# Performance work log

Measured on AMD Instinct MI355X. Metric: run time of the kernel, lower is better.

Reference implementation:

```python
import jax, jax.numpy as jnp
import numpy as np

B, QLEN, MLEN, E, H, DH = 2, 1024, 1024, 1024, 16, 64
KLEN = QLEN + MLEN
LN_EPS = 1e-3  # keras LayerNormalization default epsilon


def layer_norm(x, gamma, beta):
    mu = jnp.mean(x, axis=-1, keepdims=True)
    var = jnp.mean(jnp.square(x - mu), axis=-1, keepdims=True)
    return (x - mu) * jax.lax.rsqrt(var + LN_EPS) * gamma + beta


def rel_shift(x):
    # x: [B, H, q, k] -> standard Transformer-XL relative shift
    b, h, q, k = x.shape
    x = jnp.pad(x, ((0, 0), (0, 0), (0, 0), (1, 0)))
    x = x.reshape(b, h, k + 1, q)[:, :, 1:, :]
    return x.reshape(b, h, q, k)


def setup_inputs() -> dict:
    key = jax.random.key(0)
    ks = jax.random.split(key, 12)
    s = 0.02
    inp = {
        "w": jax.random.normal(ks[0], (B, QLEN, E), jnp.float32),
        "r": jax.random.normal(ks[1], (1, KLEN, E), jnp.float32),
        "member": jax.random.normal(ks[2], (B, MLEN, E), jnp.float32),
        # causal mask over concatenated keys: 1 = masked
        "attn_mask": (jnp.arange(KLEN)[None, :] > (jnp.arange(QLEN)[:, None] + MLEN)).astype(jnp.float32),
        "Wq": jax.random.normal(ks[3], (E, H * DH), jnp.float32) * s,
        "Wk": jax.random.normal(ks[4], (E, H * DH), jnp.float32) * s,
        "Wv": jax.random.normal(ks[5], (E, H * DH), jnp.float32) * s,
        "Wr": jax.random.normal(ks[6], (E, H * DH), jnp.float32) * s,
        "Wo": jax.random.normal(ks[7], (H * DH, E), jnp.float32) * s,
        "r_w_bias": jnp.zeros((H, DH), jnp.float32),
        "r_r_bias": jnp.zeros((H, DH), jnp.float32),
        "ln1_g": jnp.ones((E,), jnp.float32),
        "ln1_b": jnp.zeros((E,), jnp.float32),
        "W1": jax.random.normal(ks[8], (E, 4 * E), jnp.float32) * s,
        "W2": jax.random.normal(ks[9], (4 * E, E), jnp.float32) * s,
        "ln2_g": jnp.ones((E,), jnp.float32),
        "ln2_b": jnp.zeros((E,), jnp.float32),
    }
    return inp


def reference(w, r, member, attn_mask, Wq, Wk, Wv, Wr, Wo, r_w_bias, r_r_bias,
              ln1_g, ln1_b, W1, W2, ln2_g, ln2_b):
    b, qlen, e = w.shape
    h, dh = r_w_bias.shape
    cat = jnp.concatenate([member, w], axis=1)          # [B, klen, E]
    q = (cat @ Wq)[:, -qlen:]                           # [B, q, H*DH]
    k = cat @ Wk                                        # [B, klen, H*DH]
    v = cat @ Wv
    rp = (r @ Wr)[0]                                    # [klen, H*DH] (shared over batch)
    qh = q.reshape(b, qlen, h, dh)
    kh = k.reshape(b, -1, h, dh)
    vh = v.reshape(b, -1, h, dh)
    rh = rp.reshape(-1, h, dh)
    AC = jnp.einsum('bqhd,bkhd->bhqk', qh + r_w_bias, kh)
    BD = jnp.einsum('bqhd,khd->bhqk', qh + r_r_bias, rh)
    BD = rel_shift(BD)
    attn = (AC + BD) / jnp.sqrt(jnp.float32(e))         # note: scaled by sqrt(embed_size)
    m = attn_mask[None, None]                           # [1,1,q,klen]
    attn = attn * (1.0 - m) - 1e30 * m
    p = jax.nn.softmax(attn, axis=-1)
    o = jnp.einsum('bhqk,bkhd->bqhd', p, vh).reshape(b, qlen, h * dh)
    o = o @ Wo
    x = layer_norm(w + o, ln1_g, ln1_b)
    y = jax.nn.relu(x @ W1) @ W2
    return layer_norm(y + x, ln2_g, ln2_b)
```

## Files before the change

### kernel.cpp

```cpp
#include <hip/hip_runtime.h>
#include <hip/hip_bf16.h>
#include <stdint.h>

typedef __bf16 bf16x8 __attribute__((ext_vector_type(8)));
typedef float  f32x4  __attribute__((ext_vector_type(4)));

constexpr int BB   = 2;
constexpr int QL   = 1024;
constexpr int ML   = 1024;
constexpr int KL   = 2048;
constexpr int ED   = 1024;
constexpr int HH   = 16;
constexpr int FF   = 4096;
constexpr size_t MN = 2048u * 1024u;

__device__ __forceinline__ bf16x8 ld8(const __hip_bfloat16* p) {
    return *reinterpret_cast<const bf16x8*>(p);
}
__device__ __forceinline__ void st8(__hip_bfloat16* p, bf16x8 v) {
    *reinterpret_cast<bf16x8*>(p) = v;
}
__device__ __forceinline__ f32x4 mfma16(bf16x8 a, bf16x8 b, f32x4 c) {
    return __builtin_amdgcn_mfma_f32_16x16x32_bf16(a, b, c, 0, 0, 0);
}
__device__ __forceinline__ void async16(void* lds, const void* g) {
    __builtin_amdgcn_global_load_lds((__attribute__((address_space(1))) void*)g,
                                     (__attribute__((address_space(3))) void*)lds,
                                     16, 0, 0);
}

__global__ __launch_bounds__(256) void build_cat_r(const float* __restrict__ w,
                                                   const float* __restrict__ mem,
                                                   const float* __restrict__ r,
                                                   __hip_bfloat16* __restrict__ cat,
                                                   __hip_bfloat16* __restrict__ rbf) {
    const int bx = blockIdx.x;
    const float* src;
    __hip_bfloat16* dst;
    size_t g;
    if (bx < 2048) {
        size_t t = (size_t)bx * 256 + threadIdx.x;
        g = t * 8;
        int b   = (int)(g >> 21);
        int rem = (int)(g & ((1u << 21) - 1));
        int j = rem >> 10, e = rem & 1023;
        src = (j < ML) ? &mem[((size_t)b * ML + j) * ED + e]
                       : &w[((size_t)b * QL + (j - ML)) * ED + e];
        dst = &cat[g];
    } else {
        g = ((size_t)(bx - 2048) * 256 + threadIdx.x) * 8;
        src = &r[g];
        dst = &rbf[g];
    }
    float4 f0 = *(const float4*)src;
    float4 f1 = *(const float4*)(src + 4);
    union { bf16x8 v; __hip_bfloat16 h[8]; } u;
    u.h[0] = __float2bfloat16(f0.x); u.h[1] = __float2bfloat16(f0.y);
    u.h[2] = __float2bfloat16(f0.z); u.h[3] = __float2bfloat16(f0.w);
    u.h[4] = __float2bfloat16(f1.x); u.h[5] = __float2bfloat16(f1.y);
    u.h[6] = __float2bfloat16(f1.z); u.h[7] = __float2bfloat16(f1.w);
    st8(dst, u.v);
}

__global__ __launch_bounds__(256) void transpose_cast(const float* __restrict__ in,
                                                      __hip_bfloat16* __restrict__ out,
                                                      int K, int N) {
    __shared__ float tile[32][33];
    const int tx = threadIdx.x & 31, ty = threadIdx.x >> 5;
    const int n0 = blockIdx.x * 32, k0 = blockIdx.y * 32;
#pragma unroll
    for (int i = 0; i < 4; ++i)
        tile[ty + i * 8][tx] = in[(size_t)(k0 + ty + i * 8) * N + n0 + tx];
    __syncthreads();
#pragma unroll
    for (int i = 0; i < 4; ++i)
        out[(size_t)(n0 + ty + i * 8) * K + k0 + tx] = __float2bfloat16(tile[tx][ty + i * 8]);
}

__global__ __launch_bounds__(256) void tc5(const float* __restrict__ s0, const float* __restrict__ s1,
                                           const float* __restrict__ s2, const float* __restrict__ s3,
                                           const float* __restrict__ s4,
                                           __hip_bfloat16* __restrict__ wqkvT,
                                           __hip_bfloat16* __restrict__ wot) {
    __shared__ float tile[32][33];
    const int z = blockIdx.z;
    const float* in = (z == 0) ? s0 : (z == 1) ? s1 : (z == 2) ? s2 : (z == 3) ? s3 : s4;
    __hip_bfloat16* out = (z == 4) ? wot : wqkvT + (size_t)z * 1024 * 1024;
    const int tx = threadIdx.x & 31, ty = threadIdx.x >> 5;
    const int n0 = blockIdx.x * 32, k0 = blockIdx.y * 32;
#pragma unroll
    for (int i = 0; i < 4; ++i)
        tile[ty + i * 8][tx] = in[(size_t)(k0 + ty + i * 8) * 1024 + n0 + tx];
    __syncthreads();
#pragma unroll
    for (int i = 0; i < 4; ++i)
        out[(size_t)(n0 + ty + i * 8) * 1024 + k0 + tx] = __float2bfloat16(tile[tx][ty + i * 8]);
}

__global__ __launch_bounds__(256) void transpose_v(const __hip_bfloat16* __restrict__ v,
                                                   __hip_bfloat16* __restrict__ vt) {
    __shared__ __hip_bfloat16 tile[32][33];
    const int tx = threadIdx.x & 31, ty = threadIdx.x >> 5;
    const int s = blockIdx.z, b = s >> 4, h = s & 15;
    const int j0 = blockIdx.x * 32, d0 = blockIdx.y * 32;
#pragma unroll
    for (int i = 0; i < 4; ++i)
        tile[ty + i * 8][tx] =
            v[((size_t)b * KL + j0 + ty + i * 8) * 1024 + h * 64 + d0 + tx];
    __syncthreads();
#pragma unroll
    for (int i = 0; i < 4; ++i)
        vt[((size_t)s * 64 + d0 + ty + i * 8) * KL + j0 + tx] = tile[tx][ty + i * 8];
}

template <int EPI, bool SK>
__global__ __launch_bounds__(256) void gemm_bt(const __hip_bfloat16* __restrict__ A,
                                               const __hip_bfloat16* __restrict__ Bt,
                                               void* __restrict__ Cv,
                                               int N, int kLen, int lda, int ldb) {
    __shared__ __align__(16) __hip_bfloat16 sA[128 * 32];
    __shared__ __align__(16) __hip_bfloat16 sB[128 * 32];
    const int tid = threadIdx.x;
    const int lane = tid & 63;
    const int l16 = lane & 15, quad = lane >> 4;
    const int wv = tid >> 6;
    const int wm = wv >> 1, wn = wv & 1;
    const int bm = blockIdx.y * 128, bn = blockIdx.x * 128;
    const int kOff = SK ? blockIdx.z * kLen : 0;
    const int c0 = tid, c1 = 256 + tid;
    const int r0 = c0 >> 2, o0 = (c0 & 3) * 8;
    const int r1 = c1 >> 2, o1 = (c1 & 3) * 8;
    f32x4 acc[4][4] = {};
    for (int k0 = 0; k0 < kLen; k0 += 32) {
        async16(&sA[c0 * 8], A + (size_t)(bm + r0) * lda + kOff + k0 + o0);
        async16(&sA[c1 * 8], A + (size_t)(bm + r1) * lda + kOff + k0 + o1);
        async16(&sB[c0 * 8], Bt + (size_t)(bn + r0) * ldb + kOff + k0 + o0);
        async16(&sB[c1 * 8], Bt + (size_t)(bn + r1) * ldb + kOff + k0 + o1);
        __syncthreads();
        bf16x8 af[4], bfr[4];
#pragma unroll
        for (int i = 0; i < 4; ++i)
            af[i] = ld8(&sA[(wm * 64 + i * 16 + l16) * 32 + quad * 8]);
#pragma unroll
        for (int j = 0; j < 4; ++j)
            bfr[j] = ld8(&sB[(wn * 64 + j * 16 + l16) * 32 + quad * 8]);
#pragma unroll
        for (int i = 0; i < 4; ++i)
#pragma unroll
            for (int j = 0; j < 4; ++j)
                acc[i][j] = mfma16(af[i], bfr[j], acc[i][j]);
        __syncthreads();
    }
#pragma unroll
    for (int i = 0; i < 4; ++i)
#pragma unroll
        for (int j = 0; j < 4; ++j)
#pragma unroll
            for (int rg = 0; rg < 4; ++rg) {
                size_t row = bm + wm * 64 + i * 16 + quad * 4 + rg;
                size_t col = bn + wn * 64 + j * 16 + l16;
                float v = acc[i][j][rg];
                if (EPI == 0) {
                    float* C = (float*)Cv + (SK ? (size_t)blockIdx.z * MN : 0);
                    C[row * N + col] = v;
                } else {
                    __hip_bfloat16* C = (__hip_bfloat16*)Cv;
                    C[row * N + col] = __float2bfloat16(fmaxf(v, 0.f));
                }
            }
}

__global__ __launch_bounds__(256) void gemm_qkvr(const __hip_bfloat16* __restrict__ cat,
                                                 const __hip_bfloat16* __restrict__ rbf,
                                                 const __hip_bfloat16* __restrict__ Bt,
                                                 __hip_bfloat16* __restrict__ qwb,
                                                 __hip_bfloat16* __restrict__ qrb,
                                                 __hip_bfloat16* __restrict__ kbuf,
                                                 __hip_bfloat16* __restrict__ vbuf,
                                                 __hip_bfloat16* __restrict__ rpb,
                                                 const float* __restrict__ rwb,
                                                 const float* __restrict__ rrb) {
    const int bm = blockIdx.y * 128, bn = blockIdx.x * 128;
    const int region = blockIdx.x >> 3;
    if (region == 0 && (bm & 2047) < 1024) return;
    if (region == 3 && bm >= 2048) return;
    const __hip_bfloat16* A = (region == 3) ? rbf : cat;
    __shared__ __align__(16) __hip_bfloat16 sA[128 * 32];
    __shared__ __align__(16) __hip_bfloat16 sB[128 * 32];
    const int tid = threadIdx.x;
    const int lane = tid & 63;
    const int l16 = lane & 15, quad = lane >> 4;
    const int wv = tid >> 6;
    const int wm = wv >> 1, wn = wv & 1;
    const int c0 = tid, c1 = 256 + tid;
    const int r0 = c0 >> 2, o0 = (c0 & 3) * 8;
    const int r1 = c1 >> 2, o1 = (c1 & 3) * 8;
    f32x4 acc[4][4] = {};
    for (int k0 = 0; k0 < 1024; k0 += 32) {
        async16(&sA[c0 * 8], A + (size_t)(bm + r0) * 1024 + k0 + o0);
        async16(&sA[c1 * 8], A + (size_t)(bm + r1) * 1024 + k0 + o1);
        async16(&sB[c0 * 8], Bt + (size_t)(bn + r0) * 1024 + k0 + o0);
        async16(&sB[c1 * 8], Bt + (size_t)(bn + r1) * 1024 + k0 + o1);
        __syncthreads();
        bf16x8 af[4], bfr[4];
#pragma unroll
        for (int i = 0; i < 4; ++i)
            af[i] = ld8(&sA[(wm * 64 + i * 16 + l16) * 32 + quad * 8]);
#pragma unroll
        for (int j = 0; j < 4; ++j)
            bfr[j] = ld8(&sB[(wn * 64 + j * 16 + l16) * 32 + quad * 8]);
#pragma unroll
        for (int i = 0; i < 4; ++i)
#pragma unroll
            for (int j = 0; j < 4; ++j)
                acc[i][j] = mfma16(af[i], bfr[j], acc[i][j]);
        __syncthreads();
    }
#pragma unroll
    for (int j = 0; j < 4; ++j) {
        const int col = bn + wn * 64 + j * 16 + l16;
        float bw = 0.f, br = 0.f;
        if (region == 0) { bw = rwb[col]; br = rrb[col]; }
#pragma unroll
        for (int i = 0; i < 4; ++i)
#pragma unroll
            for (int rg = 0; rg < 4; ++rg) {
                const int row = bm + wm * 64 + i * 16 + quad * 4 + rg;
                const int bb = row >> 11, jr = row & 2047;
                float v = acc[i][j][rg];
                if (region == 0) {
                    size_t o = ((size_t)(bb * 1024 + (jr - 1024))) * 1024 + col;
                    qwb[o] = __float2bfloat16(v + bw);
                    qrb[o] = __float2bfloat16(v + br);
                } else if (region == 1) {
                    kbuf[((size_t)(bb * 2048 + jr)) * 1024 + (col - 1024)] = __float2bfloat16(v);
                } else if (region == 2) {
                    vbuf[((size_t)(bb * 2048 + jr)) * 1024 + (col - 2048)] = __float2bfloat16(v);
                } else {
                    rpb[(size_t)row * 1024 + (col - 3072)] = __float2bfloat16(v);
                }
            }
    }
}

__global__ __launch_bounds__(64, 3) void flash_attn5(
        const __hip_bfloat16* __restrict__ qw, const __hip_bfloat16* __restrict__ qr,
        const __hip_bfloat16* __restrict__ kbuf, const __hip_bfloat16* __restrict__ vtb,
        const __hip_bfloat16* __restrict__ rpb,
        float* __restrict__ Opart, float* __restrict__ lpart) {
    __shared__ __align__(16) __hip_bfloat16 spb[32][76];
    const int lane = threadIdx.x;
    const int l16 = lane & 15, quad = lane >> 4;
    const int id    = blockIdx.x;
    const int xcd   = id & 7;
    const int rest  = id >> 3;
    const int grp   = rest >> 7;
    const int local = rest & 127;
    const int p     = grp * 8 + xcd;
    const int b = p >> 4, h = p & 15;
    const int qi = local >> 2, chunk = local & 3;
    const int i0 = qi * 32;

    bf16x8 qaw[2][2], qar[2][2];
#pragma unroll
    for (int g = 0; g < 2; ++g)
#pragma unroll
        for (int kf = 0; kf < 2; ++kf) {
            size_t qi_ = ((size_t)(b * QL + i0 + g * 16 + l16)) * 1024 + h * 64 + kf * 32 + quad * 8;
            qaw[g][kf] = ld8(&qw[qi_]);
            qar[g][kf] = ld8(&qr[qi_]);
        }
    f32x4 oacc[2][4] = {};
    f32x4 lacc[2] = {};
    union { bf16x8 v; __hip_bfloat16 h8[8]; } ou;
#pragma unroll
    for (int j = 0; j < 8; ++j) ou.h8[j] = __float2bfloat16(l16 == 0 ? 1.f : 0.f);
    const bf16x8 onesf = ou.v;

    int srcIdx[4], selr[4];
#pragma unroll
    for (int r = 0; r < 4; ++r) {
        int s = l16 + 15 - (quad * 4 + r);
        selr[r] = s >> 4;
        srcIdx[r] = (quad * 16) | (s & 15);
    }
    const int T = (i0 + 1119) >> 6;
    const int t0 = (chunk * T) >> 2, t1 = ((chunk + 1) * T) >> 2;
    const __hip_bfloat16* kB = kbuf + (size_t)b * KL * 1024 + h * 64;
    const __hip_bfloat16* vB = vtb + ((size_t)(b * HH + h) * 64) * 2048;
    const __hip_bfloat16* rB = rpb + h * 64;

    for (int jt = t0; jt < t1; ++jt) {
        const int j0 = jt * 64;
        f32x4 sfr[2][4];
#pragma unroll
        for (int nt = 0; nt < 4; ++nt) {
            const __hip_bfloat16* kr = kB + (size_t)(j0 + nt * 16 + l16) * 1024 + quad * 8;
            bf16x8 b0 = ld8(kr);
            bf16x8 b1 = ld8(kr + 32);
#pragma unroll
            for (int g = 0; g < 2; ++g) {
                f32x4 z = {};
                z = mfma16(qaw[g][0], b0, z);
                z = mfma16(qaw[g][1], b1, z);
                sfr[g][nt] = z;
            }
        }
        f32x4 bd[2][5];
        const int ubase = j0 - i0 + 992;
#pragma unroll
        for (int s = 0; s < 6; ++s) {
            int row = ubase + s * 16 + l16;
            if (row > 2047) row = 2047;
            const __hip_bfloat16* rr = rB + (size_t)row * 1024 + quad * 8;
            bf16x8 f0 = ld8(rr);
            bf16x8 f1 = ld8(rr + 32);
            if (s >= 1) {
                f32x4 z = {};
                z = mfma16(qar[0][0], f0, z);
                z = mfma16(qar[0][1], f1, z);
                bd[0][s - 1] = z;
            }
            if (s <= 4) {
                f32x4 z = {};
                z = mfma16(qar[1][0], f0, z);
                z = mfma16(qar[1][1], f1, z);
                bd[1][s] = z;
            }
        }
#pragma unroll
        for (int g = 0; g < 2; ++g) {
            float pre[5][4];
#pragma unroll
            for (int t = 0; t < 5; ++t)
#pragma unroll
                for (int r = 0; r < 4; ++r)
                    pre[t][r] = __shfl(bd[g][t][r], srcIdx[r], 64);
#pragma unroll
            for (int nt = 0; nt < 4; ++nt)
#pragma unroll
                for (int r = 0; r < 4; ++r) {
                    float bdv = selr[r] ? pre[nt + 1][r] : pre[nt][r];
                    float sv = (sfr[g][nt][r] + bdv) * 0.03125f;
                    int ii = i0 + g * 16 + quad * 4 + r;
                    int jj = j0 + nt * 16 + l16;
                    float p_ = (jj <= ii + ML) ? __expf(sv) : 0.f;
                    spb[g * 16 + quad * 4 + r][nt * 16 + l16] = __float2bfloat16(p_);
                }
        }
        bf16x8 pa[2][2];
#pragma unroll
        for (int g = 0; g < 2; ++g) {
            pa[g][0] = ld8(&spb[g * 16 + l16][quad * 8]);
            pa[g][1] = ld8(&spb[g * 16 + l16][32 + quad * 8]);
            lacc[g] = mfma16(pa[g][0], onesf, lacc[g]);
            lacc[g] = mfma16(pa[g][1], onesf, lacc[g]);
        }
#pragma unroll
        for (int dt = 0; dt < 4; ++dt) {
            const __hip_bfloat16* vr = vB + (size_t)(dt * 16 + l16) * 2048 + j0 + quad * 8;
            bf16x8 v0 = ld8(vr);
            bf16x8 v1 = ld8(vr + 32);
#pragma unroll
            for (int g = 0; g < 2; ++g) {
                oacc[g][dt] = mfma16(pa[g][0], v0, oacc[g][dt]);
                oacc[g][dt] = mfma16(pa[g][1], v1, oacc[g][dt]);
            }
        }
    }
    const size_t obase = ((size_t)((chunk * 2 + b) * HH + h)) * (1024 * 64);
#pragma unroll
    for (int g = 0; g < 2; ++g)
#pragma unroll
        for (int dt = 0; dt < 4; ++dt)
#pragma unroll
            for (int r = 0; r < 4; ++r) {
                int q = i0 + g * 16 + quad * 4 + r;
                Opart[obase + (size_t)q * 64 + dt * 16 + l16] = oacc[g][dt][r];
            }
    if (l16 == 0) {
        const size_t lbase = ((size_t)((chunk * 2 + b) * HH + h)) * 1024;
#pragma unroll
        for (int g = 0; g < 2; ++g)
#pragma unroll
            for (int r = 0; r < 4; ++r) {
                int q = i0 + g * 16 + quad * 4 + r;
                lpart[lbase + q] = lacc[g][r];
            }
    }
}

__global__ __launch_bounds__(256) void combine_attn(const float* __restrict__ Opart,
                                                    const float* __restrict__ lpart,
                                                    __hip_bfloat16* __restrict__ og) {
    size_t t = (size_t)blockIdx.x * 256 + threadIdx.x;
    size_t e4 = t * 4;
    int d  = (int)(e4 & 63);
    int q  = (int)((e4 >> 6) & 1023);
    int hh = (int)((e4 >> 16) & 15);
    int bb = (int)(e4 >> 20);
    float ox = 0.f, oy = 0.f, oz = 0.f, ow = 0.f, l = 0.f;
#pragma unroll
    for (int c = 0; c < 4; ++c) {
        size_t gsel = (size_t)((c * 2 + bb) * HH + hh);
        float4 o = *(const float4*)&Opart[gsel * (1024 * 64) + (size_t)q * 64 + d];
        ox += o.x; oy += o.y; oz += o.z; ow += o.w;
        l += lpart[gsel * 1024 + q];
    }
    float inv = 1.f / l;
    union { __hip_bfloat16 h[4]; uint2 u; } o;
    o.h[0] = __float2bfloat16(ox * inv);
    o.h[1] = __float2bfloat16(oy * inv);
    o.h[2] = __float2bfloat16(oz * inv);
    o.h[3] = __float2bfloat16(ow * inv);
    *(uint2*)&og[((size_t)bb * 1024 + q) * 1024 + hh * 64 + d] = o.u;
}

template <int NP, bool WB>
__global__ __launch_bounds__(256) void add_ln_k(const float* __restrict__ res,
                                                const float* __restrict__ parts,
                                                const float* __restrict__ gam,
                                                const float* __restrict__ bet,
                                                float* __restrict__ of,
                                                __hip_bfloat16* __restrict__ ob) {
    const int tid = threadIdx.x;
    const size_t base = (size_t)blockIdx.x * ED;
    const int col = tid * 4;
    float4 va = *(const float4*)&res[base + col];
    float x0 = va.x, x1 = va.y, x2 = va.z, x3 = va.w;
#pragma unroll
    for (int z = 0; z < NP; ++z) {
        float4 p = *(const float4*)&parts[(size_t)z * MN + base + col];
        x0 += p.x; x1 += p.y; x2 += p.z; x3 += p.w;
    }
    float s1 = x0 + x1 + x2 + x3;
    float s2 = x0 * x0 + x1 * x1 + x2 * x2 + x3 * x3;
    for (int o = 32; o > 0; o >>= 1) {
        s1 += __shfl_down(s1, o, 64);
        s2 += __shfl_down(s2, o, 64);
    }
    __shared__ float p1[4], p2[4];
    if ((tid & 63) == 0) { p1[tid >> 6] = s1; p2[tid >> 6] = s2; }
    __syncthreads();
    float S1 = p1[0] + p1[1] + p1[2] + p1[3];
    float S2 = p2[0] + p2[1] + p2[2] + p2[3];
    float mu = S1 * (1.0f / ED);
    float var = S2 * (1.0f / ED) - mu * mu;
    float rs = rsqrtf(var + 1e-3f);
    float4 g4 = *(const float4*)&gam[col];
    float4 b4 = *(const float4*)&bet[col];
    float y0 = (x0 - mu) * rs * g4.x + b4.x;
    float y1 = (x1 - mu) * rs * g4.y + b4.y;
    float y2 = (x2 - mu) * rs * g4.z + b4.z;
    float y3 = (x3 - mu) * rs * g4.w + b4.w;
    *(float4*)&of[base + col] = make_float4(y0, y1, y2, y3);
    if (WB) {
        ob[base + col + 0] = __float2bfloat16(y0);
        ob[base + col + 1] = __float2bfloat16(y1);
        ob[base + col + 2] = __float2bfloat16(y2);
        ob[base + col + 3] = __float2bfloat16(y3);
    }
}

extern "C" void kernel_launch(void* const* d_in, const int* in_sizes, int n_in,
                              void* d_out, int out_size, void* d_ws, size_t ws_size,
                              hipStream_t stream) {
    const float* w   = (const float*)d_in[0];
    const float* r   = (const float*)d_in[1];
    const float* mem = (const float*)d_in[2];
    const float* Wq  = (const float*)d_in[4];
    const float* Wk  = (const float*)d_in[5];
    const float* Wv  = (const float*)d_in[6];
    const float* Wr  = (const float*)d_in[7];
    const float* Wo  = (const float*)d_in[8];
    const float* rwb = (const float*)d_in[9];
    const float* rrb = (const float*)d_in[10];
    const float* g1  = (const float*)d_in[11];
    const float* b1  = (const float*)d_in[12];
    const float* W1  = (const float*)d_in[13];
    const float* W2  = (const float*)d_in[14];
    const float* g2  = (const float*)d_in[15];
    const float* b2  = (const float*)d_in[16];

    char* ws = (char*)d_ws;
    size_t off = 0;
    auto alloc = [&](size_t bytes) -> void* {
        void* p = ws + off;
        off += (bytes + 255) & ~(size_t)255;
        return p;
    };
    __hip_bfloat16* wqkvT = (__hip_bfloat16*)alloc((size_t)4096 * 1024 * 2);
    __hip_bfloat16* wot   = (__hip_bfloat16*)alloc((size_t)ED * ED * 2);
    __hip_bfloat16* w1t   = (__hip_bfloat16*)alloc((size_t)FF * ED * 2);
    __hip_bfloat16* w2t   = (__hip_bfloat16*)alloc((size_t)ED * FF * 2);
    __hip_bfloat16* qwb   = (__hip_bfloat16*)alloc((size_t)BB * QL * ED * 2);
    __hip_bfloat16* qrb   = (__hip_bfloat16*)alloc((size_t)BB * QL * ED * 2);
    __hip_bfloat16* vtb   = (__hip_bfloat16*)alloc((size_t)BB * KL * ED * 2);
    __hip_bfloat16* rpb   = (__hip_bfloat16*)alloc((size_t)KL * ED * 2);
    __hip_bfloat16* og    = (__hip_bfloat16*)alloc((size_t)BB * QL * ED * 2);
    char* regA = (char*)alloc((size_t)BB * KL * ED * 2);
    __hip_bfloat16* cat = (__hip_bfloat16*)regA;
    float*          xf  = (float*)regA;
    char* regB = (char*)alloc((size_t)KL * ED * 2);
    __hip_bfloat16* rbf = (__hip_bfloat16*)regB;
    __hip_bfloat16* xb  = (__hip_bfloat16*)regB;
    char* regC = (char*)alloc((size_t)BB * QL * FF * 2);
    __hip_bfloat16* kbuf = (__hip_bfloat16*)regC;
    __hip_bfloat16* vbuf = (__hip_bfloat16*)(regC + (size_t)BB * KL * ED * 2);
    __hip_bfloat16* y1   = (__hip_bfloat16*)regC;
    const size_t opartBytes = (size_t)8 * HH * QL * 64 * 4;
    const size_t lpartBytes = (size_t)8 * HH * QL * 4;
    size_t regEsz = opartBytes + lpartBytes;
    if (regEsz < (size_t)4 * MN * 4) regEsz = (size_t)4 * MN * 4;
    char* regE = (char*)alloc(regEsz);
    float* Opart  = (float*)regE;
    float* lpart  = (float*)(regE + opartBytes);
    float* o_part = (float*)regE;
    float* f_part = (float*)regE;
    if (off > ws_size) return;

    build_cat_r<<<3072, 256, 0, stream>>>(w, mem, r, cat, rbf);
    tc5<<<dim3(32, 32, 5), 256, 0, stream>>>(Wq, Wk, Wv, Wr, Wo, wqkvT, wot);
    transpose_cast<<<dim3(128, 32), 256, 0, stream>>>(W1, w1t, 1024, 4096);
    transpose_cast<<<dim3(32, 128), 256, 0, stream>>>(W2, w2t, 4096, 1024);

    gemm_qkvr<<<dim3(32, 32), 256, 0, stream>>>(cat, rbf, wqkvT, qwb, qrb, kbuf, vbuf, rpb,
                                                rwb, rrb);
    transpose_v<<<dim3(64, 2, 32), 256, 0, stream>>>(vbuf, vtb);

    flash_attn5<<<dim3(4096), 64, 0, stream>>>(qwb, qrb, kbuf, vtb, rpb, Opart, lpart);
    combine_attn<<<2048, 256, 0, stream>>>(Opart, lpart, og);

    gemm_bt<0, true><<<dim3(8, 16, 4), 256, 0, stream>>>(og, wot, o_part, 1024, 256, 1024, 1024);
    add_ln_k<4, true><<<2048, 256, 0, stream>>>(w, o_part, g1, b1, xf, xb);

    gemm_bt<2, false><<<dim3(32, 16, 1), 256, 0, stream>>>(xb, w1t, y1, 4096, 1024, 1024, 1024);
    gemm_bt<0, true><<<dim3(8, 16, 4), 256, 0, stream>>>(y1, w2t, f_part, 1024, 1024, 4096, 4096);
    add_ln_k<4, false><<<2048, 256, 0, stream>>>(xf, f_part, g2, b2, (float*)d_out, nullptr);
}
```

Measured before the change: 454.0 us.

## Share K and relative-position tiles in LDS across two waves in flash attention

The attention kernel now runs two waves per block, each handling 32 query rows of a 64-row block. The K tile and a 128-row relative-position window are staged cooperatively in shared memory, so both waves reuse them instead of each loading from global memory. The key-range split drops from four chunks to two, which halves the partial outputs the combine step has to merge. The cost is two block-wide barriers per tile, fewer and larger blocks, and more shared memory per block, which may lower occupancy.

Result: no change. 461.0 us (+1.5%).

```diff
diff --git a/kernel.cpp b/kernel.cpp
--- a/kernel.cpp
+++ b/kernel.cpp
@@ -243,32 +243,34 @@
     }
 }
 
-__global__ __launch_bounds__(64, 3) void flash_attn5(
+__global__ __launch_bounds__(128, 2) void flash_attn6(
         const __hip_bfloat16* __restrict__ qw, const __hip_bfloat16* __restrict__ qr,
         const __hip_bfloat16* __restrict__ kbuf, const __hip_bfloat16* __restrict__ vtb,
         const __hip_bfloat16* __restrict__ rpb,
         float* __restrict__ Opart, float* __restrict__ lpart) {
-    __shared__ __align__(16) __hip_bfloat16 spb[32][76];
-    const int lane = threadIdx.x;
+    __shared__ __align__(16) __hip_bfloat16 sk[64][72];
+    __shared__ __align__(16) __hip_bfloat16 srp[128][72];
+    __shared__ __align__(16) __hip_bfloat16 spb[2][32][72];
+    const int tid = threadIdx.x, wv = tid >> 6, lane = tid & 63;
     const int l16 = lane & 15, quad = lane >> 4;
     const int id    = blockIdx.x;
     const int xcd   = id & 7;
     const int rest  = id >> 3;
-    const int grp   = rest >> 7;
-    const int local = rest & 127;
+    const int grp   = rest >> 5;
+    const int local = rest & 31;
     const int p     = grp * 8 + xcd;
     const int b = p >> 4, h = p & 15;
-    const int qi = local >> 2, chunk = local & 3;
-    const int i0 = qi * 32;
+    const int qb = local >> 1, chunk = local & 1;
+    const int i0b = qb * 64, i0w = i0b + wv * 32;
 
     bf16x8 qaw[2][2], qar[2][2];
 #pragma unroll
     for (int g = 0; g < 2; ++g)
 #pragma unroll
         for (int kf = 0; kf < 2; ++kf) {
-            size_t qi_ = ((size_t)(b * QL + i0 + g * 16 + l16)) * 1024 + h * 64 + kf * 32 + quad * 8;
-            qaw[g][kf] = ld8(&qw[qi_]);
-            qar[g][kf] = ld8(&qr[qi_]);
+            size_t qi = ((size_t)(b * QL + i0w + g * 16 + l16)) * 1024 + h * 64 + kf * 32 + quad * 8;
+            qaw[g][kf] = ld8(&qw[qi]);
+            qar[g][kf] = ld8(&qr[qi]);
         }
     f32x4 oacc[2][4] = {};
     f32x4 lacc[2] = {};
@@ -282,22 +284,45 @@
     for (int r = 0; r < 4; ++r) {
         int s = l16 + 15 - (quad * 4 + r);
         selr[r] = s >> 4;
-        srcIdx[r] = (quad * 16) | (s & 15);
-    }
-    const int T = (i0 + 1119) >> 6;
-    const int t0 = (chunk * T) >> 2, t1 = ((chunk + 1) * T) >> 2;
-    const __hip_bfloat16* kB = kbuf + (size_t)b * KL * 1024 + h * 64;
-    const __hip_bfloat16* vB = vtb + ((size_t)(b * HH + h) * 64) * 2048;
-    const __hip_bfloat16* rB = rpb + h * 64;
+        srcIdx[r] = (lane & 48) | (s & 15);
+    }
+    const int T = qb + 17, Ta = T >> 1;
+    const int t0 = chunk ? Ta : 0, t1 = chunk ? T : Ta;
+    const int rbase = 32 - wv * 32;
 
     for (int jt = t0; jt < t1; ++jt) {
         const int j0 = jt * 64;
+        const int ub = j0 - i0b + 960;
+#pragma unroll
+        for (int pp = 0; pp < 4; ++pp) {
+            int cc = pp * 128 + tid, row = cc >> 3, off = (cc & 7) * 8;
+            st8(&sk[row][off], ld8(&kbuf[((size_t)(b * KL + j0 + row)) * 1024 + h * 64 + off]));
+        }
+#pragma unroll
+        for (int pp = 0; pp < 8; ++pp) {
+            int cc = pp * 128 + tid, row = cc >> 3, off = (cc & 7) * 8;
+            int u = ub + row;
+            if (u < KL) {
+                st8(&srp[row][off], ld8(&rpb[(size_t)u * 1024 + h * 64 + off]));
+            } else {
+                union { bf16x8 v; uint32_t w[4]; } z;
+                z.w[0] = z.w[1] = z.w[2] = z.w[3] = 0u;
+                st8(&srp[row][off], z.v);
+            }
+        }
+        bf16x8 vvf[4][2];
+#pragma unroll
+        for (int dt = 0; dt < 4; ++dt) {
+            size_t vr = ((size_t)((b * HH + h) * 64 + dt * 16 + l16)) * 2048 + j0 + quad * 8;
+            vvf[dt][0] = ld8(&vtb[vr]);
+            vvf[dt][1] = ld8(&vtb[vr + 32]);
+        }
+        __syncthreads();
         f32x4 sfr[2][4];
 #pragma unroll
         for (int nt = 0; nt < 4; ++nt) {
-            const __hip_bfloat16* kr = kB + (size_t)(j0 + nt * 16 + l16) * 1024 + quad * 8;
-            bf16x8 b0 = ld8(kr);
-            bf16x8 b1 = ld8(kr + 32);
+            bf16x8 b0 = ld8(&sk[nt * 16 + l16][quad * 8]);
+            bf16x8 b1 = ld8(&sk[nt * 16 + l16][32 + quad * 8]);
 #pragma unroll
             for (int g = 0; g < 2; ++g) {
                 f32x4 z = {};
@@ -306,67 +331,55 @@
                 sfr[g][nt] = z;
             }
         }
-        f32x4 bd[2][5];
-        const int ubase = j0 - i0 + 992;
-#pragma unroll
-        for (int s = 0; s < 6; ++s) {
-            int row = ubase + s * 16 + l16;
-            if (row > 2047) row = 2047;
-            const __hip_bfloat16* rr = rB + (size_t)row * 1024 + quad * 8;
-            bf16x8 f0 = ld8(rr);
-            bf16x8 f1 = ld8(rr + 32);
-            if (s >= 1) {
+        bf16x8 bF0[6], bF1[6];
+#pragma unroll
+        for (int t = 0; t < 6; ++t) {
+            int rr = rbase + t * 16 + l16;
+            bF0[t] = ld8(&srp[rr][quad * 8]);
+            bF1[t] = ld8(&srp[rr][32 + quad * 8]);
+        }
+#pragma unroll
+        for (int g = 0; g < 2; ++g) {
+            f32x4 bd[5];
+#pragma unroll
+            for (int t = 0; t < 5; ++t) {
+                int ts = t + 1 - g;
                 f32x4 z = {};
-                z = mfma16(qar[0][0], f0, z);
-                z = mfma16(qar[0][1], f1, z);
-                bd[0][s - 1] = z;
-            }
-            if (s <= 4) {
-                f32x4 z = {};
-                z = mfma16(qar[1][0], f0, z);
-                z = mfma16(qar[1][1], f1, z);
-                bd[1][s] = z;
-            }
-        }
-#pragma unroll
-        for (int g = 0; g < 2; ++g) {
+                z = mfma16(qar[g][0], bF0[ts], z);
+                z = mfma16(qar[g][1], bF1[ts], z);
+                bd[t] = z;
+            }
             float pre[5][4];
 #pragma unroll
             for (int t = 0; t < 5; ++t)
 #pragma unroll
                 for (int r = 0; r < 4; ++r)
-                    pre[t][r] = __shfl(bd[g][t][r], srcIdx[r], 64);
+                    pre[t][r] = __shfl(bd[t][r], srcIdx[r], 64);
 #pragma unroll
             for (int nt = 0; nt < 4; ++nt)
 #pragma unroll
                 for (int r = 0; r < 4; ++r) {
                     float bdv = selr[r] ? pre[nt + 1][r] : pre[nt][r];
                     float sv = (sfr[g][nt][r] + bdv) * 0.03125f;
-                    int ii = i0 + g * 16 + quad * 4 + r;
+                    int ii = i0w + g * 16 + quad * 4 + r;
                     int jj = j0 + nt * 16 + l16;
                     float p_ = (jj <= ii + ML) ? __expf(sv) : 0.f;
-                    spb[g * 16 + quad * 4 + r][nt * 16 + l16] = __float2bfloat16(p_);
+                    spb[wv][g * 16 + quad * 4 + r][nt * 16 + l16] = __float2bfloat16(p_);
                 }
         }
-        bf16x8 pa[2][2];
 #pragma unroll
         for (int g = 0; g < 2; ++g) {
-            pa[g][0] = ld8(&spb[g * 16 + l16][quad * 8]);
-            pa[g][1] = ld8(&spb[g * 16 + l16][32 + quad * 8]);
-            lacc[g] = mfma16(pa[g][0], onesf, lacc[g]);
-            lacc[g] = mfma16(pa[g][1], onesf, lacc[g]);
-        }
-#pragma unroll
-        for (int dt = 0; dt < 4; ++dt) {
-            const __hip_bfloat16* vr = vB + (size_t)(dt * 16 + l16) * 2048 + j0 + quad * 8;
-            bf16x8 v0 = ld8(vr);
-            bf16x8 v1 = ld8(vr + 32);
-#pragma unroll
-            for (int g = 0; g < 2; ++g) {
-                oacc[g][dt] = mfma16(pa[g][0], v0, oacc[g][dt]);
-                oacc[g][dt] = mfma16(pa[g][1], v1, oacc[g][dt]);
-            }
-        }
+            bf16x8 pa0 = ld8(&spb[wv][g * 16 + l16][quad * 8]);
+            bf16x8 pa1 = ld8(&spb[wv][g * 16 + l16][32 + quad * 8]);
+            lacc[g] = mfma16(pa0, onesf, lacc[g]);
+            lacc[g] = mfma16(pa1, onesf, lacc[g]);
+#pragma unroll
+            for (int dt = 0; dt < 4; ++dt) {
+                oacc[g][dt] = mfma16(pa0, vvf[dt][0], oacc[g][dt]);
+                oacc[g][dt] = mfma16(pa1, vvf[dt][1], oacc[g][dt]);
+            }
+        }
+        __syncthreads();
     }
     const size_t obase = ((size_t)((chunk * 2 + b) * HH + h)) * (1024 * 64);
 #pragma unroll
@@ -375,7 +388,7 @@
         for (int dt = 0; dt < 4; ++dt)
 #pragma unroll
             for (int r = 0; r < 4; ++r) {
-                int q = i0 + g * 16 + quad * 4 + r;
+                int q = i0w + g * 16 + quad * 4 + r;
                 Opart[obase + (size_t)q * 64 + dt * 16 + l16] = oacc[g][dt][r];
             }
     if (l16 == 0) {
@@ -384,7 +397,7 @@
         for (int g = 0; g < 2; ++g)
 #pragma unroll
             for (int r = 0; r < 4; ++r) {
-                int q = i0 + g * 16 + quad * 4 + r;
+                int q = i0w + g * 16 + quad * 4 + r;
                 lpart[lbase + q] = lacc[g][r];
             }
     }
@@ -401,7 +414,7 @@
     int bb = (int)(e4 >> 20);
     float ox = 0.f, oy = 0.f, oz = 0.f, ow = 0.f, l = 0.f;
 #pragma unroll
-    for (int c = 0; c < 4; ++c) {
+    for (int c = 0; c < 2; ++c) {
         size_t gsel = (size_t)((c * 2 + bb) * HH + hh);
         float4 o = *(const float4*)&Opart[gsel * (1024 * 64) + (size_t)q * 64 + d];
         ox += o.x; oy += o.y; oz += o.z; ow += o.w;
@@ -508,8 +521,8 @@
     __hip_bfloat16* kbuf = (__hip_bfloat16*)regC;
     __hip_bfloat16* vbuf = (__hip_bfloat16*)(regC + (size_t)BB * KL * ED * 2);
     __hip_bfloat16* y1   = (__hip_bfloat16*)regC;
-    const size_t opartBytes = (size_t)8 * HH * QL * 64 * 4;
-    const size_t lpartBytes = (size_t)8 * HH * QL * 4;
+    const size_t opartBytes = (size_t)4 * HH * QL * 64 * 4;
+    const size_t lpartBytes = (size_t)4 * HH * QL * 4;
     size_t regEsz = opartBytes + lpartBytes;
     if (regEsz < (size_t)4 * MN * 4) regEsz = (size_t)4 * MN * 4;
     char* regE = (char*)alloc(regEsz);
@@ -528,7 +541,7 @@
                                                 rwb, rrb);
     transpose_v<<<dim3(64, 2, 32), 256, 0, stream>>>(vbuf, vtb);
 
-    flash_attn5<<<dim3(4096), 64, 0, stream>>>(qwb, qrb, kbuf, vtb, rpb, Opart, lpart);
+    flash_attn6<<<dim3(1024), 128, 0, stream>>>(qwb, qrb, kbuf, vtb, rpb, Opart, lpart);
     combine_attn<<<2048, 256, 0, stream>>>(Opart, lpart, og);
 
     gemm_bt<0, true><<<dim3(8, 16, 4), 256, 0, stream>>>(og, wot, o_part, 1024, 256, 1024, 1024);
```
